# Kernel optimization log

Hardware: AMD Instinct MI355X
Metric: run time of the kernel (lower is better)

The kernel has to match this reference:

```python
import jax, jax.numpy as jnp
import numpy as np

B, T, D = 64, 2048, 256


def setup_inputs() -> dict:
    key = jax.random.key(0)
    k0, k1, k2, k3 = jax.random.split(key, 4)
    x0 = jax.random.normal(k0, (B, D), dtype=jnp.float32)
    I = jax.random.normal(k1, (B, T, D), dtype=jnp.float32)
    # Scale transition matrix so spectral norm < 1 (stable 2048-step recurrence),
    # mimicking eW = expm((W - I)*dt/tau) which is contractive for stable W.
    eW = jax.random.normal(k2, (D, D), dtype=jnp.float32) * (0.9 / np.sqrt(D))
    W_inv_eW = jax.random.normal(k3, (D, D), dtype=jnp.float32) * (1.0 / np.sqrt(D))
    return {"x0": x0, "I": I, "eW": eW, "W_inv_eW": W_inv_eW}


def reference(x0, I, eW, W_inv_eW):
    # x[:,0]=x0; x[:,t] = x[:,t-1] @ eW.T + I[:,t-1] @ W_inv_eW.T
    u = jnp.einsum('btd,sd->bts', I, W_inv_eW)  # [B, T, D], precompute input drive

    def step(x, u_t):
        x_new = x @ eW.T + u_t  # [B, D]
        return x_new, x_new

    # only u[:, :T-1] is consumed (x[:,t] uses I[:,t-1])
    _, xs = jax.lax.scan(step, x0, jnp.swapaxes(u[:, :-1], 0, 1))  # xs: [T-1, B, D]
    x = jnp.concatenate([x0[:, None, :], jnp.swapaxes(xs, 0, 1)], axis=1)  # [B, T, D]
    return x
```

## Files before the change

### kernel.cpp

```cpp
#include <hip/hip_runtime.h>
#include <stdint.h>
#include <stddef.h>


#define BATCH 64
#define TLEN 2048
#define DDIM 256
#define CHUNK 32
#define NCHUNK 64

typedef __attribute__((ext_vector_type(8))) short short8;
typedef __attribute__((ext_vector_type(4))) float f32x4;
typedef __attribute__((ext_vector_type(16))) float f32x16;

#define MFMA16(a, b, c) __builtin_amdgcn_mfma_f32_16x16x32_bf16((a), (b), (c), 0, 0, 0)
#define MFMA32(a, b, c) __builtin_amdgcn_mfma_f32_32x32x16_bf16((a), (b), (c), 0, 0, 0)
#define PIN8(x) asm volatile("" : "+v"(x))

__device__ __forceinline__ uint16_t f2bf(float f) {
  union { float f; uint32_t u; } v; v.f = f;
  return (uint16_t)((v.u + 0x7fffu + ((v.u >> 16) & 1u)) >> 16);
}
__device__ __forceinline__ float bf2f(uint16_t h) {
  union { uint32_t u; float f; } v; v.u = ((uint32_t)h) << 16;
  return v.f;
}

__device__ __forceinline__ void split8(const float* fv, short8& hi, short8& lo) {
#pragma unroll
  for (int j = 0; j < 8; ++j) {
    uint16_t hb = f2bf(fv[j]);
    hi[j] = (short)hb;
    lo[j] = (short)f2bf(fv[j] - bf2f(hb));
  }
}

__device__ __forceinline__ uint32_t swz(int row) {
  return ((uint32_t)((row & 7) << 4)) ^ ((uint32_t)(((row >> 3) & 1) << 7));
}
__device__ __forceinline__ uint32_t swz32(int row) {
  return ((uint32_t)((row & 7) << 4)) ^ ((uint32_t)(((row >> 3) & 3) << 7));
}

__device__ __forceinline__ void wg_barrier() {
  __builtin_amdgcn_sched_barrier(0);
  asm volatile("s_waitcnt lgkmcnt(0)" ::: "memory");
  __builtin_amdgcn_s_barrier();
  asm volatile("" ::: "memory");
  __builtin_amdgcn_sched_barrier(0);
}

#define WS_M1F    (0)
#define WS_M1_HI  (256 * 1024)
#define WS_M1_LO  (384 * 1024)
#define WS_M2F    (512 * 1024)
#define WS_M2_HI  (768 * 1024)
#define WS_M2_LO  (896 * 1024)
#define WS_M3F    (1024 * 1024)
#define WS_M3_HI  (1280 * 1024)
#define WS_M3_LO  (1408 * 1024)
#define WS_S      (2560 * 1024)

__global__ __launch_bounds__(512, 1) void k_u(const float* __restrict__ I,
                                              const float* __restrict__ Wi,
                                              float* __restrict__ out) {
  const int tid = threadIdx.x;
  const int w = tid >> 6, l = tid & 63, l31 = l & 31, half = l >> 5;
  const int ns = w * 32;
  __shared__ __align__(16) uint16_t sIh[2][8192];
  __shared__ __align__(16) uint16_t sIl[2][8192];

  short8 bh[16], bl[16];
#pragma unroll
  for (int ks = 0; ks < 16; ++ks) {
    const float* wp = Wi + (size_t)(ns + l31) * 256 + ks * 16 + half * 8;
    f32x4 f0 = *reinterpret_cast<const f32x4*>(wp);
    f32x4 f1 = *reinterpret_cast<const f32x4*>(wp + 4);
    float fv[8] = {f0[0], f0[1], f0[2], f0[3], f1[0], f1[1], f1[2], f1[3]};
    split8(fv, bh[ks], bl[ks]);
    PIN8(bh[ks]);
    PIN8(bl[ks]);
  }

  const int srow = tid >> 4;
  const int sc0 = (tid & 15) * 16;
  const uint32_t wb0 = ((uint32_t)(srow * 512 + sc0 * 2)) ^ swz32(srow);
  const uint32_t wb1 = ((uint32_t)(srow * 512 + sc0 * 2 + 16)) ^ swz32(srow);

  f32x4 ra[4], rb[4];
  auto loadI = [&](int tl, f32x4 (&dst)[4]) {
    const int b = tl >> 6, tt = tl & 63;
    const float* src = I + ((size_t)b * TLEN + tt * 32 + srow) * DDIM + sc0;
#pragma unroll
    for (int j = 0; j < 4; ++j)
      dst[j] = *reinterpret_cast<const f32x4*>(src + j * 4);
  };

  auto do_tile = [&](int tl, f32x4 (&cur)[4], int q, bool pre) {
    short8 hi[2], lo[2];
#pragma unroll
    for (int h2 = 0; h2 < 2; ++h2) {
      float fv[8] = {cur[h2 * 2][0], cur[h2 * 2][1], cur[h2 * 2][2], cur[h2 * 2][3],
                     cur[h2 * 2 + 1][0], cur[h2 * 2 + 1][1], cur[h2 * 2 + 1][2], cur[h2 * 2 + 1][3]};
      split8(fv, hi[h2], lo[h2]);
    }
    if (pre) loadI(tl + 512, cur);
    *reinterpret_cast<short8*>(reinterpret_cast<char*>(sIh[q]) + wb0) = hi[0];
    *reinterpret_cast<short8*>(reinterpret_cast<char*>(sIh[q]) + wb1) = hi[1];
    *reinterpret_cast<short8*>(reinterpret_cast<char*>(sIl[q]) + wb0) = lo[0];
    *reinterpret_cast<short8*>(reinterpret_cast<char*>(sIl[q]) + wb1) = lo[1];
    wg_barrier();
    const int b = tl >> 6, tt = tl & 63;
    f32x16 acc = {0.f};
#pragma unroll
    for (int j = 0; j < 16; ++j) acc[j] = 0.f;
    __builtin_amdgcn_s_setprio(1);
#pragma unroll
    for (int ks = 0; ks < 16; ++ks) {
      uint32_t rbyte = ((uint32_t)(l31 * 512 + ks * 32 + half * 16)) ^ swz32(l31);
      short8 ih = *reinterpret_cast<const short8*>((const char*)sIh[q] + rbyte);
      short8 il = *reinterpret_cast<const short8*>((const char*)sIl[q] + rbyte);
      acc = MFMA32(ih, bh[ks], acc);
      acc = MFMA32(il, bh[ks], acc);
      acc = MFMA32(ih, bl[ks], acc);
    }
    __builtin_amdgcn_s_setprio(0);
#pragma unroll
    for (int r = 0; r < 16; ++r) {
      int row = (r & 3) + 8 * (r >> 2) + 4 * half;
      int trow = tt * 32 + row;
      if (trow <= TLEN - 2) {
        out[((size_t)b * TLEN + trow + 1) * DDIM + ns + l31] = acc[r];
      }
    }
  };

  const int tl0 = blockIdx.x;
  loadI(tl0, ra);
  loadI(tl0 + 256, rb);
#pragma unroll 1
  for (int it = 0; it < 16; it += 2) {
    do_tile(tl0 + it * 256, ra, 0, it + 2 < 16);
    do_tile(tl0 + (it + 1) * 256, rb, 1, it + 3 < 16);
  }
}

__global__ __launch_bounds__(1024) void k_scan(const int pass,
                                               const float* __restrict__ eW,
                                               float* __restrict__ xu,
                                               const float* __restrict__ x0,
                                               float* __restrict__ S,
                                               const uint16_t* __restrict__ M1h,
                                               const uint16_t* __restrict__ M1l,
                                               const uint16_t* __restrict__ M2h,
                                               const uint16_t* __restrict__ M2l) {
  const int tid = threadIdx.x;
  const int w = tid >> 6, l = tid & 63, l15 = l & 15, quad = l >> 4;
  const int ns = w * 16;
  const int c = blockIdx.x >> 2;
  const int rg = blockIdx.x & 3;
  __shared__ __align__(16) uint16_t sh[2][4096];
  __shared__ __align__(16) uint16_t sl[2][4096];

  const int t0 = c * CHUNK;
  const int nsteps = (t0 + CHUNK <= TLEN - 1) ? CHUNK : (TLEN - 1 - t0);

  float u0[4], u1[4], u2[4], u3[4], fin[4];
#pragma unroll
  for (int j = 0; j < 4; ++j) { u0[j] = 0.f; u1[j] = 0.f; u2[j] = 0.f; u3[j] = 0.f; fin[j] = 0.f; }

  auto issue_u = [&](int i, float (&dst)[4]) {
    if (i > nsteps) return;
#pragma unroll
    for (int r = 0; r < 4; ++r) {
      int b = rg * 16 + quad * 4 + r;
      dst[r] = xu[((size_t)b * TLEN + t0 + i) * DDIM + ns + l15];
    }
  };
  issue_u(1, u0);
  issue_u(2, u1);
  issue_u(3, u2);
  issue_u(4, u3);

  short8 fAh[8], fAl[8];
#pragma unroll
  for (int ks = 0; ks < 8; ++ks) {
    const float* ap = eW + (size_t)(ns + l15) * 256 + ks * 32 + quad * 8;
    f32x4 f0 = *reinterpret_cast<const f32x4*>(ap);
    f32x4 f1 = *reinterpret_cast<const f32x4*>(ap + 4);
    float fv[8] = {f0[0], f0[1], f0[2], f0[3], f1[0], f1[1], f1[2], f1[3]};
    split8(fv, fAh[ks], fAl[ks]);
    PIN8(fAh[ks]);
    PIN8(fAl[ks]);
  }

  if (pass == 1) {
    for (int i = tid; i < 4096; i += 1024) {
      int row = i >> 8, k = i & 255;
      uint32_t byte = ((uint32_t)(row * 512 + k * 2)) ^ swz(row);
      *(uint16_t*)((char*)sh[0] + byte) = 0;
      *(uint16_t*)((char*)sl[0] + byte) = 0;
    }
  } else {
    f32x4 yacc;
    {
      const float* Tc = (c == 0) ? x0 : (S + (size_t)(c - 1) * 64 * 256);
#pragma unroll
      for (int r = 0; r < 4; ++r)
        yacc[r] = Tc[(size_t)(rg * 16 + quad * 4 + r) * 256 + ns + l15];
    }
#pragma unroll 1
    for (int j = 1; j <= 2; ++j) {
      int k = c - j;
      if (k < 0) break;
      const float* Tp = (k == 0) ? x0 : (S + (size_t)(k - 1) * 64 * 256);
      const uint16_t* Bh = (j == 1) ? M1h : M2h;
      const uint16_t* Bl = (j == 1) ? M1l : M2l;
#pragma unroll
      for (int ks = 0; ks < 8; ++ks) {
        const float* ap = Tp + (size_t)(rg * 16 + l15) * 256 + ks * 32 + quad * 8;
        f32x4 f0 = *reinterpret_cast<const f32x4*>(ap);
        f32x4 f1 = *reinterpret_cast<const f32x4*>(ap + 4);
        float fv[8] = {f0[0], f0[1], f0[2], f0[3], f1[0], f1[1], f1[2], f1[3]};
        short8 ah, al8;
        split8(fv, ah, al8);
        const int off = (ns + l15) * 256 + ks * 32 + quad * 8;
        short8 bhf = *reinterpret_cast<const short8*>(Bh + off);
        short8 blf = *reinterpret_cast<const short8*>(Bl + off);
        yacc = MFMA16(ah, bhf, yacc);
        yacc = MFMA16(al8, bhf, yacc);
        yacc = MFMA16(ah, blf, yacc);
      }
    }
#pragma unroll
    for (int r = 0; r < 4; ++r) {
      int row = quad * 4 + r, col = ns + l15;
      float v = yacc[r];
      if (c == 0) xu[((size_t)(rg * 16 + row) * TLEN) * DDIM + col] = v;
      uint16_t hb = f2bf(v);
      uint16_t lb = f2bf(v - bf2f(hb));
      uint32_t byte = ((uint32_t)(row * 512 + col * 2)) ^ swz(row);
      *(uint16_t*)((char*)sh[0] + byte) = hb;
      *(uint16_t*)((char*)sl[0] + byte) = lb;
    }
  }
  wg_barrier();

  int p = 0;
  auto step = [&](int i, float (&ucur)[4]) {
    f32x4 acc = {0.f, 0.f, 0.f, 0.f};
    __builtin_amdgcn_s_setprio(1);
#pragma unroll
    for (int ks = 0; ks < 8; ++ks) {
      uint32_t byte = ((uint32_t)(l15 * 512 + ks * 64 + quad * 16)) ^ swz(l15);
      short8 xh = *reinterpret_cast<const short8*>((const char*)sh[p] + byte);
      short8 xl = *reinterpret_cast<const short8*>((const char*)sl[p] + byte);
      acc = MFMA16(xh, fAh[ks], acc);
      acc = MFMA16(xl, fAh[ks], acc);
      acc = MFMA16(xh, fAl[ks], acc);
    }
    __builtin_amdgcn_s_setprio(0);
#pragma unroll
    for (int r = 0; r < 4; ++r) fin[r] = acc[r] + ucur[r];
    issue_u(i + 4, ucur);
    if (pass == 2) {
#pragma unroll
      for (int r = 0; r < 4; ++r) {
        int b = rg * 16 + quad * 4 + r;
        xu[((size_t)b * TLEN + t0 + i) * DDIM + ns + l15] = fin[r];
      }
    }
    if (i < nsteps) {
#pragma unroll
      for (int r = 0; r < 4; ++r) {
        int row = quad * 4 + r, col = ns + l15;
        float v = fin[r];
        uint16_t hb = f2bf(v);
        uint16_t lb = f2bf(v - bf2f(hb));
        uint32_t byte = ((uint32_t)(row * 512 + col * 2)) ^ swz(row);
        *(uint16_t*)((char*)sh[p ^ 1] + byte) = hb;
        *(uint16_t*)((char*)sl[p ^ 1] + byte) = lb;
      }
      wg_barrier();
      p ^= 1;
    }
  };

  int i = 1;
  for (; i + 3 <= nsteps; i += 4) {
    step(i, u0);
    step(i + 1, u1);
    step(i + 2, u2);
    step(i + 3, u3);
  }
  if (i <= nsteps) { step(i, u0); ++i; }
  if (i <= nsteps) { step(i, u1); ++i; }
  if (i <= nsteps) { step(i, u2); ++i; }

  if (pass == 1) {
#pragma unroll
    for (int r = 0; r < 4; ++r) {
      int row = quad * 4 + r, col = ns + l15;
      S[((size_t)c * 64 + rg * 16 + row) * DDIM + col] = fin[r];
    }
  }
}

__global__ __launch_bounds__(512) void k_mm256A(const float* __restrict__ eW,
                                                float* __restrict__ Of,
                                                uint16_t* __restrict__ Oh,
                                                uint16_t* __restrict__ Ol) {
  const int mf = blockIdx.x;
  const int tid = threadIdx.x;
  const int w = tid >> 6, l = tid & 63, l15 = l & 15, quad = l >> 4;
  const int ns = w * 32;
  f32x4 acc[2];
  acc[0] = {0.f, 0.f, 0.f, 0.f};
  acc[1] = {0.f, 0.f, 0.f, 0.f};

#pragma unroll
  for (int ks = 0; ks < 8; ++ks) {
    float fv[8];
#pragma unroll
    for (int j = 0; j < 8; ++j)
      fv[j] = eW[(size_t)(ks * 32 + quad * 8 + j) * 256 + mf * 16 + l15];
    short8 ah, al8;
    split8(fv, ah, al8);
#pragma unroll
    for (int nf = 0; nf < 2; ++nf) {
      const float* bp = eW + (size_t)(ns + nf * 16 + l15) * 256 + ks * 32 + quad * 8;
      f32x4 b0 = *reinterpret_cast<const f32x4*>(bp);
      f32x4 b1 = *reinterpret_cast<const f32x4*>(bp + 4);
      float bv[8] = {b0[0], b0[1], b0[2], b0[3], b1[0], b1[1], b1[2], b1[3]};
      short8 bhf, blf;
      split8(bv, bhf, blf);
      acc[nf] = MFMA16(ah, bhf, acc[nf]);
      acc[nf] = MFMA16(al8, bhf, acc[nf]);
      acc[nf] = MFMA16(ah, blf, acc[nf]);
    }
  }
#pragma unroll
  for (int nf = 0; nf < 2; ++nf)
#pragma unroll
    for (int r = 0; r < 4; ++r) {
      int row = mf * 16 + quad * 4 + r;
      int col = ns + nf * 16 + l15;
      float v = acc[nf][r];
      Of[(size_t)row * 256 + col] = v;
      uint16_t hb = f2bf(v);
      Oh[(size_t)col * 256 + row] = hb;
      Ol[(size_t)col * 256 + row] = f2bf(v - bf2f(hb));
    }
}

__global__ __launch_bounds__(512) void k_mm256(const float* __restrict__ Af,
                                               const uint16_t* __restrict__ Bh,
                                               const uint16_t* __restrict__ Bl,
                                               float* __restrict__ Of,
                                               uint16_t* __restrict__ Oh,
                                               uint16_t* __restrict__ Ol) {
  const int mf = blockIdx.x;
  const int tid = threadIdx.x;
  const int w = tid >> 6, l = tid & 63, l15 = l & 15, quad = l >> 4;
  const int ns = w * 32;
  f32x4 acc[2];
  acc[0] = {0.f, 0.f, 0.f, 0.f};
  acc[1] = {0.f, 0.f, 0.f, 0.f};

#pragma unroll
  for (int ks = 0; ks < 8; ++ks) {
    const float* ap = Af + (size_t)(mf * 16 + l15) * 256 + ks * 32 + quad * 8;
    f32x4 f0 = *reinterpret_cast<const f32x4*>(ap);
    f32x4 f1 = *reinterpret_cast<const f32x4*>(ap + 4);
    float fv[8] = {f0[0], f0[1], f0[2], f0[3], f1[0], f1[1], f1[2], f1[3]};
    short8 ah, al8;
    split8(fv, ah, al8);
#pragma unroll
    for (int nf = 0; nf < 2; ++nf) {
      const int off = (ns + nf * 16 + l15) * 256 + ks * 32 + quad * 8;
      short8 bhf = *reinterpret_cast<const short8*>(Bh + off);
      short8 blf = *reinterpret_cast<const short8*>(Bl + off);
      acc[nf] = MFMA16(ah, bhf, acc[nf]);
      acc[nf] = MFMA16(al8, bhf, acc[nf]);
      acc[nf] = MFMA16(ah, blf, acc[nf]);
    }
  }
#pragma unroll
  for (int nf = 0; nf < 2; ++nf)
#pragma unroll
    for (int r = 0; r < 4; ++r) {
      int row = mf * 16 + quad * 4 + r;
      int col = ns + nf * 16 + l15;
      float v = acc[nf][r];
      Of[(size_t)row * 256 + col] = v;
      uint16_t hb = f2bf(v);
      Oh[(size_t)col * 256 + row] = hb;
      Ol[(size_t)col * 256 + row] = f2bf(v - bf2f(hb));
    }
}

extern "C" void kernel_launch(void* const* d_in, const int* in_sizes, int n_in,
                              void* d_out, int out_size, void* d_ws, size_t ws_size,
                              hipStream_t stream) {
  (void)in_sizes; (void)n_in; (void)out_size; (void)ws_size;
  const float* x0 = (const float*)d_in[0];
  const float* I  = (const float*)d_in[1];
  const float* eW = (const float*)d_in[2];
  const float* Wi = (const float*)d_in[3];
  float* out = (float*)d_out;
  char* ws = (char*)d_ws;

  float*    M1f = (float*)(ws + WS_M1F);
  uint16_t* M1h = (uint16_t*)(ws + WS_M1_HI);
  uint16_t* M1l = (uint16_t*)(ws + WS_M1_LO);
  float*    M2f = (float*)(ws + WS_M2F);
  uint16_t* M2h = (uint16_t*)(ws + WS_M2_HI);
  uint16_t* M2l = (uint16_t*)(ws + WS_M2_LO);
  float*    M3f = (float*)(ws + WS_M3F);
  uint16_t* M3h = (uint16_t*)(ws + WS_M3_HI);
  uint16_t* M3l = (uint16_t*)(ws + WS_M3_LO);
  float*    S   = (float*)(ws + WS_S);

  k_u<<<256, 512, 0, stream>>>(I, Wi, out);
  k_mm256A<<<16, 512, 0, stream>>>(eW, M3f, M3h, M3l);
  k_mm256<<<16, 512, 0, stream>>>(M3f, M3h, M3l, M2f, M2h, M2l);
  k_mm256<<<16, 512, 0, stream>>>(M2f, M2h, M2l, M3f, M3h, M3l);
  k_mm256<<<16, 512, 0, stream>>>(M3f, M3h, M3l, M2f, M2h, M2l);
  k_mm256<<<16, 512, 0, stream>>>(M2f, M2h, M2l, M1f, M1h, M1l);
  k_mm256<<<16, 512, 0, stream>>>(M1f, M1h, M1l, M2f, M2h, M2l);
  k_scan<<<256, 1024, 0, stream>>>(1, eW, out, x0, S, M1h, M1l, M2h, M2l);
  k_scan<<<256, 1024, 0, stream>>>(2, eW, out, x0, S, M1h, M1l, M2h, M2l);
}
```

Baseline: 282.4 us.

## Fold matrix-power chain into extra block of input-projection kernel

Removes the six separate launches that build the eW power matrices. An extra 257th workgroup of k_u now computes them serially, with block-level syncs between stages, while the other 256 blocks compute the input drive. This hides the launch overhead and the small serial GEMM chain behind k_u. The cost is that this single block does 16x more work per stage on one CU, which could become the critical path and make k_u longer.

```diff
diff --git a/kernel.cpp b/kernel.cpp
--- a/kernel.cpp
+++ b/kernel.cpp
@@ -61,11 +61,109 @@
 #define WS_M3_LO  (1408 * 1024)
 #define WS_S      (2560 * 1024)
 
-__global__ __launch_bounds__(512, 1) void k_u(const float* __restrict__ I,
-                                              const float* __restrict__ Wi,
-                                              float* __restrict__ out) {
+__global__ __launch_bounds__(512, 1) void k_u(
+    const float* __restrict__ I, const float* __restrict__ Wi,
+    float* __restrict__ out, const float* __restrict__ eW,
+    float* __restrict__ M1f, uint16_t* __restrict__ M1h, uint16_t* __restrict__ M1l,
+    float* __restrict__ M2f, uint16_t* __restrict__ M2h, uint16_t* __restrict__ M2l,
+    float* __restrict__ M3f, uint16_t* __restrict__ M3h, uint16_t* __restrict__ M3l) {
   const int tid = threadIdx.x;
   const int w = tid >> 6, l = tid & 63, l31 = l & 31, half = l >> 5;
+
+  if (blockIdx.x == 256) {
+    const int l15 = l & 15, quad = l >> 4;
+    const int ns = w * 32;
+
+    auto mmstage = [&](const float* Af, const uint16_t* Bh, const uint16_t* Bl,
+                       float* Of, uint16_t* Oh, uint16_t* Ol) {
+#pragma unroll 1
+      for (int mf = 0; mf < 16; ++mf) {
+        f32x4 acc[2];
+        acc[0] = {0.f, 0.f, 0.f, 0.f};
+        acc[1] = {0.f, 0.f, 0.f, 0.f};
+#pragma unroll
+        for (int ks = 0; ks < 8; ++ks) {
+          const float* ap = Af + (size_t)(mf * 16 + l15) * 256 + ks * 32 + quad * 8;
+          f32x4 f0 = *reinterpret_cast<const f32x4*>(ap);
+          f32x4 f1 = *reinterpret_cast<const f32x4*>(ap + 4);
+          float fv[8] = {f0[0], f0[1], f0[2], f0[3], f1[0], f1[1], f1[2], f1[3]};
+          short8 ah, al8;
+          split8(fv, ah, al8);
+#pragma unroll
+          for (int nf = 0; nf < 2; ++nf) {
+            const int off = (ns + nf * 16 + l15) * 256 + ks * 32 + quad * 8;
+            short8 bhf = *reinterpret_cast<const short8*>(Bh + off);
+            short8 blf = *reinterpret_cast<const short8*>(Bl + off);
+            acc[nf] = MFMA16(ah, bhf, acc[nf]);
+            acc[nf] = MFMA16(al8, bhf, acc[nf]);
+            acc[nf] = MFMA16(ah, blf, acc[nf]);
+          }
+        }
+#pragma unroll
+        for (int nf = 0; nf < 2; ++nf)
+#pragma unroll
+          for (int r = 0; r < 4; ++r) {
+            int row = mf * 16 + quad * 4 + r;
+            int col = ns + nf * 16 + l15;
+            float v = acc[nf][r];
+            Of[(size_t)row * 256 + col] = v;
+            uint16_t hb = f2bf(v);
+            Oh[(size_t)col * 256 + row] = hb;
+            Ol[(size_t)col * 256 + row] = f2bf(v - bf2f(hb));
+          }
+      }
+      __syncthreads();
+    };
+
+#pragma unroll 1
+    for (int mf = 0; mf < 16; ++mf) {
+      f32x4 acc[2];
+      acc[0] = {0.f, 0.f, 0.f, 0.f};
+      acc[1] = {0.f, 0.f, 0.f, 0.f};
+#pragma unroll
+      for (int ks = 0; ks < 8; ++ks) {
+        float fv[8];
+#pragma unroll
+        for (int j = 0; j < 8; ++j)
+          fv[j] = eW[(size_t)(ks * 32 + quad * 8 + j) * 256 + mf * 16 + l15];
+        short8 ah, al8;
+        split8(fv, ah, al8);
+#pragma unroll
+        for (int nf = 0; nf < 2; ++nf) {
+          const float* bp = eW + (size_t)(ns + nf * 16 + l15) * 256 + ks * 32 + quad * 8;
+          f32x4 b0 = *reinterpret_cast<const f32x4*>(bp);
+          f32x4 b1 = *reinterpret_cast<const f32x4*>(bp + 4);
+          float bv[8] = {b0[0], b0[1], b0[2], b0[3], b1[0], b1[1], b1[2], b1[3]};
+          short8 bhf, blf;
+          split8(bv, bhf, blf);
+          acc[nf] = MFMA16(ah, bhf, acc[nf]);
+          acc[nf] = MFMA16(al8, bhf, acc[nf]);
+          acc[nf] = MFMA16(ah, blf, acc[nf]);
+        }
+      }
+#pragma unroll
+      for (int nf = 0; nf < 2; ++nf)
+#pragma unroll
+        for (int r = 0; r < 4; ++r) {
+          int row = mf * 16 + quad * 4 + r;
+          int col = ns + nf * 16 + l15;
+          float v = acc[nf][r];
+          M3f[(size_t)row * 256 + col] = v;
+          uint16_t hb = f2bf(v);
+          M3h[(size_t)col * 256 + row] = hb;
+          M3l[(size_t)col * 256 + row] = f2bf(v - bf2f(hb));
+        }
+    }
+    __syncthreads();
+
+    mmstage(M3f, M3h, M3l, M2f, M2h, M2l);
+    mmstage(M2f, M2h, M2l, M3f, M3h, M3l);
+    mmstage(M3f, M3h, M3l, M2f, M2h, M2l);
+    mmstage(M2f, M2h, M2l, M1f, M1h, M1l);
+    mmstage(M1f, M1h, M1l, M2f, M2h, M2l);
+    return;
+  }
+
   const int ns = w * 32;
   __shared__ __align__(16) uint16_t sIh[2][8192];
   __shared__ __align__(16) uint16_t sIl[2][8192];
@@ -111,7 +209,7 @@
     *reinterpret_cast<short8*>(reinterpret_cast<char*>(sIl[q]) + wb1) = lo[1];
     wg_barrier();
     const int b = tl >> 6, tt = tl & 63;
-    f32x16 acc = {0.f};
+    f32x16 acc;
 #pragma unroll
     for (int j = 0; j < 16; ++j) acc[j] = 0.f;
     __builtin_amdgcn_s_setprio(1);
@@ -306,99 +404,6 @@
   }
 }
 
-__global__ __launch_bounds__(512) void k_mm256A(const float* __restrict__ eW,
-                                                float* __restrict__ Of,
-                                                uint16_t* __restrict__ Oh,
-                                                uint16_t* __restrict__ Ol) {
-  const int mf = blockIdx.x;
-  const int tid = threadIdx.x;
-  const int w = tid >> 6, l = tid & 63, l15 = l & 15, quad = l >> 4;
-  const int ns = w * 32;
-  f32x4 acc[2];
-  acc[0] = {0.f, 0.f, 0.f, 0.f};
-  acc[1] = {0.f, 0.f, 0.f, 0.f};
-
-#pragma unroll
-  for (int ks = 0; ks < 8; ++ks) {
-    float fv[8];
-#pragma unroll
-    for (int j = 0; j < 8; ++j)
-      fv[j] = eW[(size_t)(ks * 32 + quad * 8 + j) * 256 + mf * 16 + l15];
-    short8 ah, al8;
-    split8(fv, ah, al8);
-#pragma unroll
-    for (int nf = 0; nf < 2; ++nf) {
-      const float* bp = eW + (size_t)(ns + nf * 16 + l15) * 256 + ks * 32 + quad * 8;
-      f32x4 b0 = *reinterpret_cast<const f32x4*>(bp);
-      f32x4 b1 = *reinterpret_cast<const f32x4*>(bp + 4);
-      float bv[8] = {b0[0], b0[1], b0[2], b0[3], b1[0], b1[1], b1[2], b1[3]};
-      short8 bhf, blf;
-      split8(bv, bhf, blf);
-      acc[nf] = MFMA16(ah, bhf, acc[nf]);
-      acc[nf] = MFMA16(al8, bhf, acc[nf]);
-      acc[nf] = MFMA16(ah, blf, acc[nf]);
-    }
-  }
-#pragma unroll
-  for (int nf = 0; nf < 2; ++nf)
-#pragma unroll
-    for (int r = 0; r < 4; ++r) {
-      int row = mf * 16 + quad * 4 + r;
-      int col = ns + nf * 16 + l15;
-      float v = acc[nf][r];
-      Of[(size_t)row * 256 + col] = v;
-      uint16_t hb = f2bf(v);
-      Oh[(size_t)col * 256 + row] = hb;
-      Ol[(size_t)col * 256 + row] = f2bf(v - bf2f(hb));
-    }
-}
-
-__global__ __launch_bounds__(512) void k_mm256(const float* __restrict__ Af,
-                                               const uint16_t* __restrict__ Bh,
-                                               const uint16_t* __restrict__ Bl,
-                                               float* __restrict__ Of,
-                                               uint16_t* __restrict__ Oh,
-                                               uint16_t* __restrict__ Ol) {
-  const int mf = blockIdx.x;
-  const int tid = threadIdx.x;
-  const int w = tid >> 6, l = tid & 63, l15 = l & 15, quad = l >> 4;
-  const int ns = w * 32;
-  f32x4 acc[2];
-  acc[0] = {0.f, 0.f, 0.f, 0.f};
-  acc[1] = {0.f, 0.f, 0.f, 0.f};
-
-#pragma unroll
-  for (int ks = 0; ks < 8; ++ks) {
-    const float* ap = Af + (size_t)(mf * 16 + l15) * 256 + ks * 32 + quad * 8;
-    f32x4 f0 = *reinterpret_cast<const f32x4*>(ap);
-    f32x4 f1 = *reinterpret_cast<const f32x4*>(ap + 4);
-    float fv[8] = {f0[0], f0[1], f0[2], f0[3], f1[0], f1[1], f1[2], f1[3]};
-    short8 ah, al8;
-    split8(fv, ah, al8);
-#pragma unroll
-    for (int nf = 0; nf < 2; ++nf) {
-      const int off = (ns + nf * 16 + l15) * 256 + ks * 32 + quad * 8;
-      short8 bhf = *reinterpret_cast<const short8*>(Bh + off);
-      short8 blf = *reinterpret_cast<const short8*>(Bl + off);
-      acc[nf] = MFMA16(ah, bhf, acc[nf]);
-      acc[nf] = MFMA16(al8, bhf, acc[nf]);
-      acc[nf] = MFMA16(ah, blf, acc[nf]);
-    }
-  }
-#pragma unroll
-  for (int nf = 0; nf < 2; ++nf)
-#pragma unroll
-    for (int r = 0; r < 4; ++r) {
-      int row = mf * 16 + quad * 4 + r;
-      int col = ns + nf * 16 + l15;
-      float v = acc[nf][r];
-      Of[(size_t)row * 256 + col] = v;
-      uint16_t hb = f2bf(v);
-      Oh[(size_t)col * 256 + row] = hb;
-      Ol[(size_t)col * 256 + row] = f2bf(v - bf2f(hb));
-    }
-}
-
 extern "C" void kernel_launch(void* const* d_in, const int* in_sizes, int n_in,
                               void* d_out, int out_size, void* d_ws, size_t ws_size,
                               hipStream_t stream) {
@@ -421,13 +426,8 @@
   uint16_t* M3l = (uint16_t*)(ws + WS_M3_LO);
   float*    S   = (float*)(ws + WS_S);
 
-  k_u<<<256, 512, 0, stream>>>(I, Wi, out);
-  k_mm256A<<<16, 512, 0, stream>>>(eW, M3f, M3h, M3l);
-  k_mm256<<<16, 512, 0, stream>>>(M3f, M3h, M3l, M2f, M2h, M2l);
-  k_mm256<<<16, 512, 0, stream>>>(M2f, M2h, M2l, M3f, M3h, M3l);
-  k_mm256<<<16, 512, 0, stream>>>(M3f, M3h, M3l, M2f, M2h, M2l);
-  k_mm256<<<16, 512, 0, stream>>>(M2f, M2h, M2l, M1f, M1h, M1l);
-  k_mm256<<<16, 512, 0, stream>>>(M1f, M1h, M1l, M2f, M2h, M2l);
+  k_u<<<257, 512, 0, stream>>>(I, Wi, out, eW,
+                               M1f, M1h, M1l, M2f, M2h, M2l, M3f, M3h, M3l);
   k_scan<<<256, 1024, 0, stream>>>(1, eW, out, x0, S, M1h, M1l, M2h, M2l);
   k_scan<<<256, 1024, 0, stream>>>(2, eW, out, x0, S, M1h, M1l, M2h, M2l);
 }
```

Measured after the change: 654.2 us. +131.7%, slower.
